# Performance work log

Hardware: AMD Instinct MI355X
Metric: run time of the kernel (lower is better)

Reference implementation:

```python
import jax, jax.numpy as jnp
import numpy as np

T = 2097152          # total points across all diagrams (per side)
N_DGM = 256          # number of diagrams
D_IN, D_HID, D_OUT = 2, 32, 32


def setup_inputs() -> dict:
    key = jax.random.key(0)
    ks = jax.random.split(key, 12)
    s = 0.3
    inp = {
        "points_t": jax.random.normal(ks[0], (T, D_IN), jnp.float32),
        "points_s": jax.random.normal(ks[1], (T, D_IN), jnp.float32),
        "w1_w": jax.random.normal(ks[2], (D_IN, D_HID), jnp.float32) * s,
        "w1_b": jax.random.normal(ks[3], (D_HID,), jnp.float32) * s,
        "w2_w": jax.random.normal(ks[4], (D_HID, 1), jnp.float32) * s,
        "w2_b": jax.random.normal(ks[5], (1,), jnp.float32) * s,
        "e1_w": jax.random.normal(ks[6], (D_IN, D_HID), jnp.float32) * s,
        "e1_b": jax.random.normal(ks[7], (D_HID,), jnp.float32) * s,
        "e2_w": jax.random.normal(ks[8], (D_HID, D_OUT), jnp.float32) * s,
        "e2_b": jax.random.normal(ks[9], (D_OUT,), jnp.float32) * s,
        "seg_t": jnp.sort(jax.random.randint(ks[10], (T,), 0, N_DGM, jnp.int32)),
        "seg_s": jnp.sort(jax.random.randint(ks[11], (T,), 0, N_DGM, jnp.int32)),
        "num_diagrams": N_DGM,
    }
    return inp


def _point_pool(pts, seg, w1_w, w1_b, w2_w, w2_b, e1_w, e1_b, e2_w, e2_b, n_dgm):
    # torch.nan_to_num(dgm, posinf=0)
    x = jnp.nan_to_num(pts, posinf=0.0)
    # weight MLP: Linear(2,32) -> ReLU -> Linear(32,1)
    w = jax.nn.relu(x @ w1_w + w1_b) @ w2_w + w2_b            # [T, 1]
    # embedding MLP: Linear(2,32) -> ReLU -> Linear(32,32)
    e = jax.nn.relu(x @ e1_w + e1_b) @ e2_w + e2_b            # [T, 32]
    prod = w * e                                              # [T, 32]
    sums = jax.ops.segment_sum(prod, seg, num_segments=n_dgm)               # [N, 32]
    cnts = jax.ops.segment_sum(jnp.ones((pts.shape[0], 1), prod.dtype), seg,
                               num_segments=n_dgm)                          # [N, 1]
    pooled = sums / jnp.maximum(cnts, 1.0)                    # per-diagram mean
    return pooled.reshape(-1)                                 # torch.cat -> [N*32]


def reference(points_t, points_s, w1_w, w1_b, w2_w, w2_b, e1_w, e1_b, e2_w, e2_b,
              seg_t, seg_s, num_diagrams):
    params = (w1_w, w1_b, w2_w, w2_b, e1_w, e1_b, e2_w, e2_b)
    emb_t = _point_pool(points_t, seg_t, *params, num_diagrams)
    emb_s = _point_pool(points_s, seg_s, *params, num_diagrams)
    return jnp.mean((emb_s - emb_t) ** 2)
```

## Files before the change

### kernel.cpp

```cpp
#include <hip/hip_runtime.h>

typedef float v2f __attribute__((ext_vector_type(2)));
typedef float f4 __attribute__((ext_vector_type(4)));

#define NSEG 256
#define BPS 4
#define KPT 4


__global__ void bounds_kernel(const int* __restrict__ seg_t,
                              const int* __restrict__ seg_s,
                              int* __restrict__ starts_t,
                              int* __restrict__ starts_s, int T) {
  int i = blockIdx.x * blockDim.x + threadIdx.x;
  const int* seg = blockIdx.y ? seg_s : seg_t;
  int* starts = blockIdx.y ? starts_s : starts_t;
  if (i >= T) return;
  int s = seg[i];
  if (i == 0) {
    for (int t = 0; t <= s; ++t) starts[t] = 0;
  } else {
    int p = seg[i - 1];
    if (p != s) {
      for (int t = p + 1; t <= s; ++t) starts[t] = i;
    }
  }
  if (i == T - 1) {
    for (int t = s + 1; t <= NSEG; ++t) starts[t] = T;
  }
}

__global__ __launch_bounds__(256, 4) void pool_kernel(
    const float2* __restrict__ pts_t, const float2* __restrict__ pts_s,
    const int* __restrict__ starts_t, const int* __restrict__ starts_s,
    const float* __restrict__ w1_w, const float* __restrict__ w1_b,
    const float* __restrict__ w2_w, const float* __restrict__ w2_b,
    const float* __restrict__ e1_w, const float* __restrict__ e1_b,
    float* __restrict__ accg, float* __restrict__ accw) {
  const int side = blockIdx.z;
  const float2* pts = side ? pts_s : pts_t;
  const int* starts = side ? starts_s : starts_t;
  const int s = blockIdx.x;
  const int tid = threadIdx.x;

  __shared__ __align__(16) float wt[16][16];
  __shared__ float w2b_sh;
  if (tid < 16) {
    const int h0 = 2 * tid, h1 = 2 * tid + 1;
    wt[tid][0] = w1_w[h0];
    wt[tid][1] = w1_w[h1];
    wt[tid][2] = w1_w[32 + h0];
    wt[tid][3] = w1_w[32 + h1];
    wt[tid][4] = w1_b[h0];
    wt[tid][5] = w1_b[h1];
    wt[tid][6] = w2_w[h0];
    wt[tid][7] = w2_w[h1];
    wt[tid][8] = e1_w[h0];
    wt[tid][9] = e1_w[h1];
    wt[tid][10] = e1_w[32 + h0];
    wt[tid][11] = e1_w[32 + h1];
    wt[tid][12] = e1_b[h0];
    wt[tid][13] = e1_b[h1];
    wt[tid][14] = 0.f;
    wt[tid][15] = 0.f;
  }
  if (tid == 0) w2b_sh = w2_b[0];
  __syncthreads();

  const int st = starts[s];
  const int en = starts[s + 1];
  const int total = en - st;
  const float w2b = w2b_sh;

  v2f ag2[16];
#pragma unroll
  for (int hp = 0; hp < 16; ++hp) ag2[hp] = (v2f)(0.f);
  float aw = 0.f;

  for (int base = ((int)blockIdx.y * 256 + tid) * KPT; base < total;
       base += BPS * 256 * KPT) {
    const int i0 = st + base;

    float px[KPT], py[KPT];
#pragma unroll
    for (int k = 0; k < KPT; ++k) {
      int ik = i0 + k;
      ik = ik < en ? ik : en - 1;
      const float2 p = pts[ik];
      px[k] = p.x;
      py[k] = p.y;
    }

    unsigned zoff = 0;
    asm volatile("" : "+v"(zoff));
    const char* wb = (const char*)(&wt[0][0]) + zoff;

    v2f wacc2[KPT];
#pragma unroll
    for (int k = 0; k < KPT; ++k) wacc2[k] = (v2f)(0.f);

#pragma unroll
    for (int hp = 0; hp < 16; ++hp) {
      const f4 qa = *(const f4*)(wb + hp * 64);
      const f4 qb = *(const f4*)(wb + hp * 64 + 16);
      const v2f ax = {qa.x, qa.y}, ay = {qa.z, qa.w};
      const v2f b1 = {qb.x, qb.y}, w22 = {qb.z, qb.w};
#pragma unroll
      for (int k = 0; k < KPT; ++k) {
        v2f t = __builtin_elementwise_fma((v2f)(py[k]), ay, b1);
        t = __builtin_elementwise_fma((v2f)(px[k]), ax, t);
        t = __builtin_elementwise_max(t, (v2f)(0.f));
        wacc2[k] = __builtin_elementwise_fma(t, w22, wacc2[k]);
      }
    }

    float wv[KPT];
#pragma unroll
    for (int k = 0; k < KPT; ++k) {
      float w = wacc2[k].x + wacc2[k].y + w2b;
      w = (i0 + k < en) ? w : 0.f;
      wv[k] = w;
      aw += w;
    }

#pragma unroll
    for (int hp = 0; hp < 16; ++hp) {
      const f4 qc = *(const f4*)(wb + hp * 64 + 32);
      const v2f ex = {qc.x, qc.y}, ey = {qc.z, qc.w};
      const v2f eb = *(const v2f*)(wb + hp * 64 + 48);
      v2f acc = ag2[hp];
#pragma unroll
      for (int k = 0; k < KPT; ++k) {
        v2f t = __builtin_elementwise_fma((v2f)(py[k]), ey, eb);
        t = __builtin_elementwise_fma((v2f)(px[k]), ex, t);
        t = __builtin_elementwise_max(t, (v2f)(0.f));
        acc = __builtin_elementwise_fma((v2f)(wv[k]), t, acc);
      }
      ag2[hp] = acc;
    }
  }

  float v[32];
#pragma unroll
  for (int hp = 0; hp < 16; ++hp) {
    v[2 * hp] = ag2[hp].x;
    v[2 * hp + 1] = ag2[hp].y;
  }
  const int l = tid & 63;

#define FOLD(M, HALF)                              \
  {                                                \
    const bool hi = (l & (M)) != 0;                \
    _Pragma("unroll") for (int i = 0; i < (HALF); ++i) { \
      const float sent = hi ? v[i] : v[i + (HALF)]; \
      const float kept = hi ? v[i + (HALF)] : v[i]; \
      v[i] = kept + __shfl_xor(sent, (M));         \
    }                                              \
  }
  FOLD(1, 16)
  FOLD(2, 8)
  FOLD(4, 4)
  FOLD(8, 2)
  FOLD(16, 1)
#undef FOLD
  v[0] += __shfl_xor(v[0], 32);
  const int h =
      ((l & 1) << 4) | ((l & 2) << 2) | (l & 4) | ((l & 8) >> 2) | ((l & 16) >> 4);

#pragma unroll
  for (int m = 1; m < 64; m <<= 1) aw += __shfl_xor(aw, m);

  const int sbase = (side * NSEG + s) * 32;
  if (l < 32) atomicAdd(&accg[sbase + h], v[0]);
  if (l == 0) atomicAdd(&accw[side * NSEG + s], aw);
}

__global__ __launch_bounds__(256) void finish_kernel(
    const float* __restrict__ accg, const float* __restrict__ accw,
    const int* __restrict__ starts_t, const int* __restrict__ starts_s,
    const float* __restrict__ e2_w, const float* __restrict__ e2_b,
    float* __restrict__ out) {
  const int s = threadIdx.x;
  __shared__ float e2s[32][33];
  __shared__ float e2bs[32];
  for (int k = threadIdx.x; k < 1024; k += 256) e2s[k >> 5][k & 31] = e2_w[k];
  if (threadIdx.x < 32) e2bs[threadIdx.x] = e2_b[threadIdx.x];
  __syncthreads();

  const float* gt = &accg[s * 32];
  const float* gs = &accg[(NSEG + s) * 32];
  const float awt = accw[s];
  const float aws = accw[NSEG + s];
  const float ct = fmaxf((float)(starts_t[s + 1] - starts_t[s]), 1.f);
  const float cs = fmaxf((float)(starts_s[s + 1] - starts_s[s]), 1.f);

  float gtl[32], gsl[32];
#pragma unroll
  for (int h = 0; h < 32; ++h) {
    gtl[h] = gt[h];
    gsl[h] = gs[h];
  }

  float part = 0.f;
#pragma unroll
  for (int o = 0; o < 32; ++o) {
    float pt = awt * e2bs[o];
    float ps = aws * e2bs[o];
#pragma unroll
    for (int h = 0; h < 32; ++h) {
      const float w = e2s[h][o];
      pt = fmaf(gtl[h], w, pt);
      ps = fmaf(gsl[h], w, ps);
    }
    pt /= ct;
    ps /= cs;
    const float d = ps - pt;
    part = fmaf(d, d, part);
  }

  __shared__ float red[256];
  red[threadIdx.x] = part;
  __syncthreads();
  for (int k = 128; k > 0; k >>= 1) {
    if (threadIdx.x < k) red[threadIdx.x] += red[threadIdx.x + k];
    __syncthreads();
  }
  if (threadIdx.x == 0) out[0] = red[0] / (float)(NSEG * 32);
}

extern "C" void kernel_launch(void* const* d_in, const int* in_sizes, int n_in,
                              void* d_out, int out_size, void* d_ws,
                              size_t ws_size, hipStream_t stream) {
  const float2* pts_t = (const float2*)d_in[0];
  const float2* pts_s = (const float2*)d_in[1];
  const float* w1_w = (const float*)d_in[2];
  const float* w1_b = (const float*)d_in[3];
  const float* w2_w = (const float*)d_in[4];
  const float* w2_b = (const float*)d_in[5];
  const float* e1_w = (const float*)d_in[6];
  const float* e1_b = (const float*)d_in[7];
  const float* e2_w = (const float*)d_in[8];
  const float* e2_b = (const float*)d_in[9];
  const int* seg_t = (const int*)d_in[10];
  const int* seg_s = (const int*)d_in[11];
  const int T = in_sizes[0] / 2;

  char* ws = (char*)d_ws;
  float* accg = (float*)ws;
  float* accw = (float*)(ws + 65536);
  int* starts_t = (int*)(ws + 67584);
  int* starts_s = (int*)(ws + 68612);

  hipMemsetAsync(d_ws, 0, 67584, stream);

  dim3 gA((T + 255) / 256, 2, 1);
  bounds_kernel<<<gA, 256, 0, stream>>>(seg_t, seg_s, starts_t, starts_s, T);

  dim3 gB(NSEG, BPS, 2);
  pool_kernel<<<gB, 256, 0, stream>>>(pts_t, pts_s, starts_t, starts_s, w1_w,
                                      w1_b, w2_w, w2_b, e1_w, e1_b, accg, accw);

  finish_kernel<<<1, 256, 0, stream>>>(accg, accw, starts_t, starts_s, e2_w,
                                       e2_b, (float*)d_out);
}
```

Baseline: 57.06 us.

## Pack weights in a prep kernel, load points as pairs, raise KPT

Adds a small kernel that packs MLP weights into a global blob, so pool blocks read them directly instead of staging through shared memory behind a barrier. Points are loaded two at a time with 16-byte loads from an even-aligned start, with validity masking against the true segment range. Points per thread rise from four to six to amortise weight loads. This trades LDS reads for global or cache reads and raises register pressure, plus one extra launch.

```diff
diff --git a/kernel.cpp b/kernel.cpp
--- a/kernel.cpp
+++ b/kernel.cpp
@@ -5,7 +5,7 @@
 
 #define NSEG 256
 #define BPS 4
-#define KPT 4
+#define KPT 6
 
 
 __global__ void bounds_kernel(const int* __restrict__ seg_t,
@@ -30,70 +30,78 @@
   }
 }
 
+__global__ void pack_kernel(const float* __restrict__ w1_w,
+                            const float* __restrict__ w1_b,
+                            const float* __restrict__ w2_w,
+                            const float* __restrict__ w2_b,
+                            const float* __restrict__ e1_w,
+                            const float* __restrict__ e1_b,
+                            float* __restrict__ blob) {
+  const int t = threadIdx.x;
+  if (t < 16) {
+    const int h0 = 2 * t, h1 = 2 * t + 1;
+    float* b = blob + t * 16;
+    b[0] = w1_w[h0];
+    b[1] = w1_w[h1];
+    b[2] = w1_w[32 + h0];
+    b[3] = w1_w[32 + h1];
+    b[4] = w1_b[h0];
+    b[5] = w1_b[h1];
+    b[6] = w2_w[h0];
+    b[7] = w2_w[h1];
+    b[8] = e1_w[h0];
+    b[9] = e1_w[h1];
+    b[10] = e1_w[32 + h0];
+    b[11] = e1_w[32 + h1];
+    b[12] = e1_b[h0];
+    b[13] = e1_b[h1];
+    b[14] = (t == 0) ? w2_b[0] : 0.f;
+    b[15] = 0.f;
+  }
+}
+
 __global__ __launch_bounds__(256, 4) void pool_kernel(
     const float2* __restrict__ pts_t, const float2* __restrict__ pts_s,
     const int* __restrict__ starts_t, const int* __restrict__ starts_s,
-    const float* __restrict__ w1_w, const float* __restrict__ w1_b,
-    const float* __restrict__ w2_w, const float* __restrict__ w2_b,
-    const float* __restrict__ e1_w, const float* __restrict__ e1_b,
-    float* __restrict__ accg, float* __restrict__ accw) {
+    const float* __restrict__ wblob, float* __restrict__ accg,
+    float* __restrict__ accw, int T) {
   const int side = blockIdx.z;
   const float2* pts = side ? pts_s : pts_t;
   const int* starts = side ? starts_s : starts_t;
   const int s = blockIdx.x;
   const int tid = threadIdx.x;
 
-  __shared__ __align__(16) float wt[16][16];
-  __shared__ float w2b_sh;
-  if (tid < 16) {
-    const int h0 = 2 * tid, h1 = 2 * tid + 1;
-    wt[tid][0] = w1_w[h0];
-    wt[tid][1] = w1_w[h1];
-    wt[tid][2] = w1_w[32 + h0];
-    wt[tid][3] = w1_w[32 + h1];
-    wt[tid][4] = w1_b[h0];
-    wt[tid][5] = w1_b[h1];
-    wt[tid][6] = w2_w[h0];
-    wt[tid][7] = w2_w[h1];
-    wt[tid][8] = e1_w[h0];
-    wt[tid][9] = e1_w[h1];
-    wt[tid][10] = e1_w[32 + h0];
-    wt[tid][11] = e1_w[32 + h1];
-    wt[tid][12] = e1_b[h0];
-    wt[tid][13] = e1_b[h1];
-    wt[tid][14] = 0.f;
-    wt[tid][15] = 0.f;
-  }
-  if (tid == 0) w2b_sh = w2_b[0];
-  __syncthreads();
-
   const int st = starts[s];
   const int en = starts[s + 1];
-  const int total = en - st;
-  const float w2b = w2b_sh;
+  const int st2 = st & ~1;
+  const int total2 = en - st2;
+  const int Tm2 = T - 2;
+  const unsigned cnt = (unsigned)(en - st);
 
   v2f ag2[16];
 #pragma unroll
   for (int hp = 0; hp < 16; ++hp) ag2[hp] = (v2f)(0.f);
-  float aw = 0.f;
-
-  for (int base = ((int)blockIdx.y * 256 + tid) * KPT; base < total;
+  v2f aw2 = (v2f)(0.f);
+
+  for (int base = ((int)blockIdx.y * 256 + tid) * KPT; base < total2;
        base += BPS * 256 * KPT) {
-    const int i0 = st + base;
-
-    float px[KPT], py[KPT];
-#pragma unroll
-    for (int k = 0; k < KPT; ++k) {
-      int ik = i0 + k;
-      ik = ik < en ? ik : en - 1;
-      const float2 p = pts[ik];
-      px[k] = p.x;
-      py[k] = p.y;
+    const int i0 = st2 + base;
+
+    v2f pxp[KPT], pyp[KPT];
+#pragma unroll
+    for (int j = 0; j < KPT / 2; ++j) {
+      int ip = i0 + 2 * j;
+      ip = ip > Tm2 ? Tm2 : ip;
+      const f4 q = *reinterpret_cast<const f4*>(&pts[ip]);
+      pxp[2 * j] = (v2f){q.x, q.x};
+      pyp[2 * j] = (v2f){q.y, q.y};
+      pxp[2 * j + 1] = (v2f){q.z, q.z};
+      pyp[2 * j + 1] = (v2f){q.w, q.w};
     }
 
     unsigned zoff = 0;
     asm volatile("" : "+v"(zoff));
-    const char* wb = (const char*)(&wt[0][0]) + zoff;
+    const char* wb = (const char*)wblob + zoff;
 
     v2f wacc2[KPT];
 #pragma unroll
@@ -107,34 +115,36 @@
       const v2f b1 = {qb.x, qb.y}, w22 = {qb.z, qb.w};
 #pragma unroll
       for (int k = 0; k < KPT; ++k) {
-        v2f t = __builtin_elementwise_fma((v2f)(py[k]), ay, b1);
-        t = __builtin_elementwise_fma((v2f)(px[k]), ax, t);
+        v2f t = __builtin_elementwise_fma(pyp[k], ay, b1);
+        t = __builtin_elementwise_fma(pxp[k], ax, t);
         t = __builtin_elementwise_max(t, (v2f)(0.f));
         wacc2[k] = __builtin_elementwise_fma(t, w22, wacc2[k]);
       }
     }
 
-    float wv[KPT];
+    const float w2b = *(const float*)(wb + 56);
+    v2f wvp[KPT];
 #pragma unroll
     for (int k = 0; k < KPT; ++k) {
       float w = wacc2[k].x + wacc2[k].y + w2b;
-      w = (i0 + k < en) ? w : 0.f;
-      wv[k] = w;
-      aw += w;
+      const bool valid = (unsigned)(i0 + k - st) < cnt;
+      w = valid ? w : 0.f;
+      wvp[k] = (v2f){w, w};
+      aw2 += wvp[k];
     }
 
 #pragma unroll
     for (int hp = 0; hp < 16; ++hp) {
       const f4 qc = *(const f4*)(wb + hp * 64 + 32);
+      const v2f eb = *(const v2f*)(wb + hp * 64 + 48);
       const v2f ex = {qc.x, qc.y}, ey = {qc.z, qc.w};
-      const v2f eb = *(const v2f*)(wb + hp * 64 + 48);
       v2f acc = ag2[hp];
 #pragma unroll
       for (int k = 0; k < KPT; ++k) {
-        v2f t = __builtin_elementwise_fma((v2f)(py[k]), ey, eb);
-        t = __builtin_elementwise_fma((v2f)(px[k]), ex, t);
+        v2f t = __builtin_elementwise_fma(pyp[k], ey, eb);
+        t = __builtin_elementwise_fma(pxp[k], ex, t);
         t = __builtin_elementwise_max(t, (v2f)(0.f));
-        acc = __builtin_elementwise_fma((v2f)(wv[k]), t, acc);
+        acc = __builtin_elementwise_fma(wvp[k], t, acc);
       }
       ag2[hp] = acc;
     }
@@ -146,16 +156,17 @@
     v[2 * hp] = ag2[hp].x;
     v[2 * hp + 1] = ag2[hp].y;
   }
+  float aw = aw2.x;
   const int l = tid & 63;
 
-#define FOLD(M, HALF)                              \
-  {                                                \
-    const bool hi = (l & (M)) != 0;                \
+#define FOLD(M, HALF)                                    \
+  {                                                      \
+    const bool hi = (l & (M)) != 0;                      \
     _Pragma("unroll") for (int i = 0; i < (HALF); ++i) { \
-      const float sent = hi ? v[i] : v[i + (HALF)]; \
-      const float kept = hi ? v[i + (HALF)] : v[i]; \
-      v[i] = kept + __shfl_xor(sent, (M));         \
-    }                                              \
+      const float sent = hi ? v[i] : v[i + (HALF)];      \
+      const float kept = hi ? v[i + (HALF)] : v[i];      \
+      v[i] = kept + __shfl_xor(sent, (M));               \
+    }                                                    \
   }
   FOLD(1, 16)
   FOLD(2, 8)
@@ -164,8 +175,8 @@
   FOLD(16, 1)
 #undef FOLD
   v[0] += __shfl_xor(v[0], 32);
-  const int h =
-      ((l & 1) << 4) | ((l & 2) << 2) | (l & 4) | ((l & 8) >> 2) | ((l & 16) >> 4);
+  const int h = ((l & 1) << 4) | ((l & 2) << 2) | (l & 4) | ((l & 8) >> 2) |
+                ((l & 16) >> 4);
 
 #pragma unroll
   for (int m = 1; m < 64; m <<= 1) aw += __shfl_xor(aw, m);
@@ -250,15 +261,17 @@
   float* accw = (float*)(ws + 65536);
   int* starts_t = (int*)(ws + 67584);
   int* starts_s = (int*)(ws + 68612);
+  float* wblob = (float*)(ws + 69696);
 
   hipMemsetAsync(d_ws, 0, 67584, stream);
 
   dim3 gA((T + 255) / 256, 2, 1);
   bounds_kernel<<<gA, 256, 0, stream>>>(seg_t, seg_s, starts_t, starts_s, T);
+  pack_kernel<<<1, 64, 0, stream>>>(w1_w, w1_b, w2_w, w2_b, e1_w, e1_b, wblob);
 
   dim3 gB(NSEG, BPS, 2);
-  pool_kernel<<<gB, 256, 0, stream>>>(pts_t, pts_s, starts_t, starts_s, w1_w,
-                                      w1_b, w2_w, w2_b, e1_w, e1_b, accg, accw);
+  pool_kernel<<<gB, 256, 0, stream>>>(pts_t, pts_s, starts_t, starts_s, wblob,
+                                      accg, accw, T);
 
   finish_kernel<<<1, 256, 0, stream>>>(accg, accw, starts_t, starts_s, e2_w,
                                        e2_b, (float*)d_out);
```

New measurement: 98.19 us. 72.1% more time.
